# Kernel optimization log

Measured on AMD Instinct MI355X. Metric: run time of the kernel, lower is better.

## Reference

```python
import jax, jax.numpy as jnp
import numpy as np

N_E = 8192
E_DIM = 256
BETA = 0.25


def setup_inputs() -> dict:
    key = jax.random.key(0)
    k1, k2 = jax.random.split(key)
    z = jax.random.normal(k1, (16, 1024, E_DIM), dtype=jnp.float32)
    # matches embedding.weight.data.uniform_(-1/n_e, 1/n_e)
    embedding = jax.random.uniform(k2, (N_E, E_DIM), dtype=jnp.float32,
                                   minval=-1.0 / N_E, maxval=1.0 / N_E)
    return {"z": z, "embedding": embedding}


def reference(z, embedding):
    B, S, D = z.shape  # [16, 1024, 256]
    zf = z.reshape(-1, D)  # [N, D], N = B*S
    # squared L2 distances to every codebook entry: [N, n_e]
    d = (jnp.sum(zf * zf, axis=1, keepdims=True)
         + jnp.sum(embedding * embedding, axis=1)
         - 2.0 * (zf @ embedding.T))
    min_encoding_indices = jnp.argmin(d, axis=1)  # [N]
    # one-hot encodings (returned by the module) [N, n_e]
    min_encodings = jax.nn.one_hot(min_encoding_indices, N_E, dtype=jnp.float32)
    # z_q = min_encodings @ embedding == gather of nearest codes
    z_q = embedding[min_encoding_indices].reshape(z.shape)  # [B, S, D]
    sg = jax.lax.stop_gradient
    loss = jnp.mean((sg(z_q) - z) ** 2) + BETA * jnp.mean((z_q - sg(z)) ** 2)
    # straight-through estimator
    z_q_st = z + sg(z_q - z)
    e_mean = jnp.mean(min_encodings, axis=0)  # [n_e]
    perplexity = jnp.exp(-jnp.sum(e_mean * jnp.log(e_mean + 1e-10)))
    return (loss, z_q_st, perplexity, min_encodings, min_encoding_indices[:, None])
```

## Files before the change

kernel.cpp:

```cpp
#include <hip/hip_runtime.h>
#include <cstddef>

#define NROWS 16384
#define NE    8192
#define DD    256

typedef unsigned long long u64;
typedef float vf4 __attribute__((ext_vector_type(4)));
typedef short bf16x8 __attribute__((ext_vector_type(8)));
typedef float f32x4 __attribute__((ext_vector_type(4)));
typedef unsigned short us8 __attribute__((ext_vector_type(8)));

#define OH_TOT ((size_t)NROWS * NE)
#define OH_VEC ((OH_TOT - 4) / 4)
#define CAND_CAP 4000000
#define LLIST_CAP 2048

__global__ __launch_bounds__(256) void k_rowsq(
    const float* __restrict__ z, const float* __restrict__ emb,
    float* __restrict__ zsq, float* __restrict__ esq,
    u64* __restrict__ best, int* __restrict__ counts,
    float* __restrict__ wadd, int* __restrict__ cand_n,
    unsigned short* __restrict__ ebf)
{
  const int g = blockIdx.x * 256 + threadIdx.x;
  if (g == 0) *cand_n = 0;
  if (g < NE) counts[g] = 0;
  if (g < NROWS) best[g] = ~0ull;

  const float* row;
  float* outp;
  if (g < NROWS) { row = z + (size_t)g * DD;            outp = zsq + g; }
  else           { row = emb + (size_t)(g - NROWS) * DD; outp = esq + (g - NROWS); }

  float sa = 0.0f;
  float half_s[2];
#pragma unroll
  for (int h = 0; h < 2; ++h) {
    const float* p = row + h * 128;
    float r[8];
    {
      const float4 v0 = *(const float4*)(p);
      const float4 v1 = *(const float4*)(p + 4);
      const float xs[8] = {v0.x, v0.y, v0.z, v0.w, v1.x, v1.y, v1.z, v1.w};
#pragma unroll
      for (int j = 0; j < 8; ++j) {
        float sq = xs[j] * xs[j];
        asm volatile("" : "+v"(sq));
        r[j] = sq;
        sa += fabsf(xs[j]);
      }
    }
    for (int i = 8; i < 128; i += 8) {
      const float4 v0 = *(const float4*)(p + i);
      const float4 v1 = *(const float4*)(p + i + 4);
      const float xs[8] = {v0.x, v0.y, v0.z, v0.w, v1.x, v1.y, v1.z, v1.w};
#pragma unroll
      for (int j = 0; j < 8; ++j) {
        float sq = xs[j] * xs[j];
        asm volatile("" : "+v"(sq));
        r[j] = r[j] + sq;
        sa += fabsf(xs[j]);
      }
    }
    half_s[h] = ((r[0] + r[1]) + (r[2] + r[3])) + ((r[4] + r[5]) + (r[6] + r[7]));
  }
  const float zs = half_s[0] + half_s[1];
  *outp = zs;
  if (g < NROWS) {
    wadd[g] = 2.0f * ((zs + 2.0f) * 1.2e-7f + 2.0f * (1.0e-6f * sa) + 5.0e-8f);
  } else {
    const int c = g - NROWS;
    const int t = c >> 4, l = c & 15;
#pragma unroll
    for (int kt = 0; kt < 8; ++kt) {
#pragma unroll
      for (int kq = 0; kq < 4; ++kq) {
        const float4 v0 = *(const float4*)(row + kt * 32 + kq * 8);
        const float4 v1 = *(const float4*)(row + kt * 32 + kq * 8 + 4);
        const float xs[8] = {v0.x, v0.y, v0.z, v0.w, v1.x, v1.y, v1.z, v1.w};
        us8 u;
#pragma unroll
        for (int j = 0; j < 8; ++j) {
          const unsigned b = __float_as_uint(xs[j]);
          u[j] = (unsigned short)((b + 0x7FFFu + ((b >> 16) & 1u)) >> 16);
        }
        *(us8*)(ebf + (((size_t)(t * 8 + kt)) * 64 + kq * 16 + l) * 8) = u;
      }
    }
  }
}

__device__ __forceinline__ unsigned short f2bf_rne(float f) {
  const unsigned u = __float_as_uint(f);
  return (unsigned short)((u + 0x7FFFu + ((u >> 16) & 1u)) >> 16);
}
__device__ __forceinline__ unsigned encf(float f) {
  const unsigned u = __float_as_uint(f);
  return (u & 0x80000000u) ? ~u : (u | 0x80000000u);
}
__device__ __forceinline__ float decf(unsigned k) {
  const unsigned u = (k & 0x80000000u) ? (k ^ 0x80000000u) : ~k;
  return __uint_as_float(u);
}

__global__ __launch_bounds__(256) void k_screen(
    const float* __restrict__ z, const unsigned short* __restrict__ ebf,
    const float* __restrict__ esq, const float* __restrict__ wadd,
    unsigned* __restrict__ cand, int* __restrict__ cand_n,
    float* __restrict__ ohbase)
{
  __shared__ unsigned smin[64];
  __shared__ float wl[64];
  __shared__ unsigned llist[LLIST_CAP];
  __shared__ unsigned lcnt;
  __shared__ unsigned gbase;

  const int tid = threadIdx.x;
  const int b = blockIdx.x;
  const int x = b & 7;
  const int quarter = x >> 1;
  const int panel = (b >> 3) * 2 + (x & 1);
  const int R0 = panel * 64;
  const int C0 = quarter * 2048;
  const int T0 = C0 >> 4;

  const int wave = tid >> 6;
  const int lane = tid & 63;
  const int l15 = lane & 15;
  const int kg = lane >> 4;

  if (tid < 64) { smin[tid] = 0xFFFFFFFFu; wl[tid] = wadd[R0 + tid]; }
  if (tid == 0) lcnt = 0;

  bf16x8 af[8];
  {
    const float* zp_ = z + (size_t)(R0 + wave * 16 + l15) * DD + kg * 8;
#pragma unroll
    for (int kt = 0; kt < 8; ++kt) {
      const float4 a0 = *(const float4*)(zp_ + kt * 32);
      const float4 a1 = *(const float4*)(zp_ + kt * 32 + 4);
      bf16x8 w;
      w[0] = (short)f2bf_rne(a0.x); w[1] = (short)f2bf_rne(a0.y);
      w[2] = (short)f2bf_rne(a0.z); w[3] = (short)f2bf_rne(a0.w);
      w[4] = (short)f2bf_rne(a1.x); w[5] = (short)f2bf_rne(a1.y);
      w[6] = (short)f2bf_rne(a1.z); w[7] = (short)f2bf_rne(a1.w);
      af[kt] = w;
    }
  }
  __syncthreads();

  const int rbase = wave * 16 + kg * 4;
  float wlr[4], thr[4], rm[4];
#pragma unroll
  for (int r = 0; r < 4; ++r) { wlr[r] = wl[rbase + r]; thr[r] = 1e30f; rm[r] = 1e30f; }

#define PUSH(E_)                                                            \
  {                                                                         \
    const unsigned s_ = atomicAdd(&lcnt, 1u);                               \
    if (s_ < LLIST_CAP) llist[s_] = (E_);                                   \
    else { const int g_ = atomicAdd(cand_n, 1);                             \
           if (g_ < CAND_CAP) cand[g_] = (E_); }                            \
  }

#define STEPBODY(S_, EMIT_)                                                 \
  {                                                                         \
    const int t0 = T0 + 2 * (S_);                                           \
    const bf16x8* fb = (const bf16x8*)ebf;                                  \
    bf16x8 b0[8], b1[8];                                                    \
    _Pragma("unroll")                                                       \
    for (int kt = 0; kt < 8; ++kt) {                                        \
      b0[kt] = fb[(size_t)(t0 * 8 + kt) * 64 + lane];                       \
      b1[kt] = fb[(size_t)((t0 + 1) * 8 + kt) * 64 + lane];                 \
    }                                                                       \
    f32x4 e0 = (f32x4){0,0,0,0}, o0 = (f32x4){0,0,0,0};                     \
    f32x4 e1 = (f32x4){0,0,0,0}, o1 = (f32x4){0,0,0,0};                     \
    _Pragma("unroll")                                                       \
    for (int kt = 0; kt < 8; kt += 2) {                                     \
      e0 = __builtin_amdgcn_mfma_f32_16x16x32_bf16(af[kt], b0[kt], e0, 0, 0, 0);         \
      o0 = __builtin_amdgcn_mfma_f32_16x16x32_bf16(af[kt + 1], b0[kt + 1], o0, 0, 0, 0); \
      e1 = __builtin_amdgcn_mfma_f32_16x16x32_bf16(af[kt], b1[kt], e1, 0, 0, 0);         \
      o1 = __builtin_amdgcn_mfma_f32_16x16x32_bf16(af[kt + 1], b1[kt + 1], o1, 0, 0, 0); \
    }                                                                       \
    const int c0 = C0 + (S_) * 32 + l15;                                    \
    const int c1 = c0 + 16;                                                 \
    const float ev0 = esq[c0];                                              \
    const float ev1 = esq[c1];                                              \
    float rv0[4], rv1[4];                                                   \
    float gm = 1e30f;                                                       \
    _Pragma("unroll")                                                       \
    for (int r = 0; r < 4; ++r) {                                           \
      rv0[r] = ev0 - 2.0f * (e0[r] + o0[r]);                                \
      rv1[r] = ev1 - 2.0f * (e1[r] + o1[r]);                                \
      const float mn = fminf(rv0[r], rv1[r]);                               \
      rm[r] = fminf(rm[r], mn);                                             \
      gm = fminf(gm, mn - thr[r]);                                          \
    }                                                                       \
    if ((EMIT_) && gm <= 0.0f) {                                            \
      _Pragma("unroll")                                                     \
      for (int r = 0; r < 4; ++r) {                                         \
        if (rv0[r] <= thr[r]) PUSH(((unsigned)(R0 + rbase + r) << 13) | (unsigned)c0); \
        if (rv1[r] <= thr[r]) PUSH(((unsigned)(R0 + rbase + r) << 13) | (unsigned)c1); \
      }                                                                     \
    }                                                                       \
  }

#define FLUSH_REFRESH                                                       \
  {                                                                         \
    _Pragma("unroll")                                                       \
    for (int r = 0; r < 4; ++r) {                                           \
      float mn = rm[r];                                                     \
      mn = fminf(mn, __shfl_xor(mn, 1, 16));                                \
      mn = fminf(mn, __shfl_xor(mn, 2, 16));                                \
      mn = fminf(mn, __shfl_xor(mn, 4, 16));                                \
      mn = fminf(mn, __shfl_xor(mn, 8, 16));                                \
      if (l15 == 0) atomicMin(&smin[rbase + r], encf(mn));                  \
    }                                                                       \
    _Pragma("unroll")                                                       \
    for (int r = 0; r < 4; ++r) thr[r] = decf(smin[rbase + r]) + wlr[r];    \
  }

#pragma unroll 1
  for (int s = 0; s < 64; ++s) {
    STEPBODY(s, (s >= 2));
    if (s == 1 || (s & 7) == 7) FLUSH_REFRESH;
  }

  __syncthreads();
#pragma unroll
  for (int r = 0; r < 4; ++r) thr[r] = decf(smin[rbase + r]) + wlr[r];
  STEPBODY(0, 1);
  STEPBODY(1, 1);

  __syncthreads();
  const unsigned n = (lcnt < LLIST_CAP) ? lcnt : LLIST_CAP;
  if (tid == 0) gbase = (unsigned)atomicAdd(cand_n, (int)n);
  __syncthreads();
  for (unsigned i = tid; i < n; i += 256) {
    const unsigned g = gbase + i;
    if (g < CAND_CAP) cand[g] = llist[i];
  }

  {
    const vf4 zz = {0.0f, 0.0f, 0.0f, 0.0f};
    float* zp0 = ohbase + 2;
    size_t zt = (size_t)b * 32768 + tid;
#pragma unroll 4
    for (int i = 0; i < 128; ++i) {
      if (zt < OH_VEC) __builtin_nontemporal_store(zz, (vf4*)(zp0 + 4 * zt));
      zt += 256;
    }
    if (b == 0 && tid == 0) { ohbase[0] = 0.0f; ohbase[1] = 0.0f; }
    if (b == 1023 && tid == 0) { ohbase[OH_TOT - 2] = 0.0f; ohbase[OH_TOT - 1] = 0.0f; }
  }
}

__global__ __launch_bounds__(256) void k_recheck(
    const float* __restrict__ z, const float* __restrict__ emb,
    const float* __restrict__ zsq, const float* __restrict__ esq,
    const unsigned* __restrict__ cand, const int* __restrict__ cand_n,
    u64* __restrict__ best)
{
  const int n = min(*cand_n, CAND_CAP);
  for (int i = blockIdx.x * 256 + threadIdx.x; i < n; i += gridDim.x * 256) {
    const unsigned e = cand[i];
    const int row = (int)(e >> 13);
    const int col = (int)(e & (NE - 1));
    const float4* zr = (const float4*)(z + (size_t)row * DD);
    const float4* er = (const float4*)(emb + (size_t)col * DD);
    float dot = 0.0f;
#pragma unroll 8
    for (int q = 0; q < 64; ++q) {
      const float4 a = zr[q];
      const float4 b = er[q];
      dot = fmaf(a.x, b.x, dot);
      dot = fmaf(a.y, b.y, dot);
      dot = fmaf(a.z, b.z, dot);
      dot = fmaf(a.w, b.w, dot);
    }
    const float s1 = zsq[row] + esq[col];
    const float dv = s1 - 2.0f * dot;
    atomicMin(&best[row], ((u64)__float_as_uint(dv) << 32) | (unsigned)col);
  }
}

__global__ __launch_bounds__(256) void k_gather2(
    const float* __restrict__ z, const float* __restrict__ emb,
    const u64* __restrict__ best,
    float* __restrict__ out_zq, float* __restrict__ out_onehot,
    float* __restrict__ out_idx, float* __restrict__ partials,
    int* __restrict__ counts)
{
  __shared__ float sred[256];
  const int row = blockIdx.x * 4 + (threadIdx.x >> 6);
  const int lane = threadIdx.x & 63;
  const int idx = (int)(unsigned)(best[row] & 0xffffffffull);
  const int k0 = lane * 4;

  const float4 e  = *(const float4*)(emb + (size_t)idx * DD + k0);
  const float4 zv = *(const float4*)(z + (size_t)row * DD + k0);
  *(float4*)(out_zq + (size_t)row * DD + k0) = e;

  const float dx = e.x - zv.x, dy = e.y - zv.y, dz = e.z - zv.z, dw = e.w - zv.w;
  sred[threadIdx.x] = dx * dx + dy * dy + dz * dz + dw * dw;

  if (lane == 0) {
    out_idx[row] = (float)idx;
    out_onehot[(size_t)row * NE + idx] = 1.0f;
    atomicAdd(&counts[idx], 1);
  }
  __syncthreads();
  for (int s = 128; s > 0; s >>= 1) {
    if (threadIdx.x < s) sred[threadIdx.x] += sred[threadIdx.x + s];
    __syncthreads();
  }
  if (threadIdx.x == 0) partials[blockIdx.x] = sred[0];
}

__global__ __launch_bounds__(256) void k_final(
    const int* __restrict__ counts, const float* __restrict__ partials,
    float* __restrict__ out_loss, float* __restrict__ out_perp)
{
  __shared__ float sred[256];
  __shared__ float sl[256];
  float le = 0.0f;
  for (int e = threadIdx.x; e < NE; e += 256) {
    const float p = (float)counts[e] * (1.0f / 16384.0f);
    le += p * logf(p + 1e-10f);
  }
  float ll = 0.0f;
  for (int b = threadIdx.x; b < NROWS / 4; b += 256) ll += partials[b];
  sred[threadIdx.x] = le;
  sl[threadIdx.x] = ll;
  __syncthreads();
  for (int s = 128; s > 0; s >>= 1) {
    if (threadIdx.x < s) {
      sred[threadIdx.x] += sred[threadIdx.x + s];
      sl[threadIdx.x] += sl[threadIdx.x + s];
    }
    __syncthreads();
  }
  if (threadIdx.x == 0) {
    *out_perp = expf(-sred[0]);
    *out_loss = sl[0] * (1.25f / 4194304.0f);
  }
}

extern "C" void kernel_launch(void* const* d_in, const int* in_sizes, int n_in,
                              void* d_out, int out_size, void* d_ws, size_t ws_size,
                              hipStream_t stream) {
  const float* z   = (const float*)d_in[0];
  const float* emb = (const float*)d_in[1];

  float* out        = (float*)d_out;
  float* out_loss   = out;
  float* out_zq     = out + 1;
  float* out_perp   = out + 4194305;
  float* out_onehot = out + 4194306;
  float* out_idx    = out + 138412034;

  float* zsq      = (float*)d_ws;
  float* esq      = zsq + NROWS;
  u64*   best     = (u64*)(esq + NE);
  int*   counts   = (int*)(best + NROWS);
  float* partials = (float*)(counts + NE);
  float* wadd     = partials + 4096;
  int*   cand_n   = (int*)(wadd + NROWS);
  unsigned short* ebf = (unsigned short*)(wadd + NROWS + 4);
  unsigned* cand  = (unsigned*)(ebf + (size_t)NE * DD);

  k_rowsq<<<96, 256, 0, stream>>>(z, emb, zsq, esq, best, counts, wadd, cand_n, ebf);
  k_screen<<<1024, 256, 0, stream>>>(z, ebf, esq, wadd, cand, cand_n, out_onehot);
  k_recheck<<<512, 256, 0, stream>>>(z, emb, zsq, esq, cand, cand_n, best);
  k_gather2<<<NROWS / 4, 256, 0, stream>>>(z, emb, best, out_zq, out_onehot,
                                           out_idx, partials, counts);
  k_final<<<1, 256, 0, stream>>>(counts, partials, out_loss, out_perp);
}
```

Before: 1.013 ms.

## Use two-pass min-then-screen in k_screen and split one-hot zeroing into kernel

The screening kernel becomes two passes. The first pass computes each row's exact block-local bf16 minimum over all 2048 columns, and the second pass recomputes the MFMA distances and emits candidates against that final threshold. This replaces the old interleaved refresh-and-emit scheme, which emitted extra candidates early while thresholds were still loose and ran two redo steps at the end. Zeroing the large one-hot output moves into a separate k_zero kernel, and waves_per_eu(3) is set on the screen kernel. The cost is doubled MFMA and codebook-read work in screening and an extra kernel launch, traded for fewer candidates to recheck.

```diff
diff --git a/kernel.cpp b/kernel.cpp
--- a/kernel.cpp
+++ b/kernel.cpp
@@ -104,11 +104,12 @@
   return __uint_as_float(u);
 }
 
-__global__ __launch_bounds__(256) void k_screen(
+__global__ __launch_bounds__(256)
+__attribute__((amdgpu_waves_per_eu(3)))
+void k_screen(
     const float* __restrict__ z, const unsigned short* __restrict__ ebf,
     const float* __restrict__ esq, const float* __restrict__ wadd,
-    unsigned* __restrict__ cand, int* __restrict__ cand_n,
-    float* __restrict__ ohbase)
+    unsigned* __restrict__ cand, int* __restrict__ cand_n)
 {
   __shared__ unsigned smin[64];
   __shared__ float wl[64];
@@ -151,9 +152,40 @@
   __syncthreads();
 
   const int rbase = wave * 16 + kg * 4;
-  float wlr[4], thr[4], rm[4];
-#pragma unroll
-  for (int r = 0; r < 4; ++r) { wlr[r] = wl[rbase + r]; thr[r] = 1e30f; rm[r] = 1e30f; }
+  const bf16x8* fb = (const bf16x8*)ebf;
+
+  float rm[4] = {1e30f, 1e30f, 1e30f, 1e30f};
+#pragma unroll 1
+  for (int tt = 0; tt < 128; ++tt) {
+    bf16x8 bfr[8];
+#pragma unroll
+    for (int kt = 0; kt < 8; ++kt)
+      bfr[kt] = fb[(size_t)((T0 + tt) * 8 + kt) * 64 + lane];
+    f32x4 e = (f32x4){0, 0, 0, 0}, o = (f32x4){0, 0, 0, 0};
+#pragma unroll
+    for (int kt = 0; kt < 8; kt += 2) {
+      e = __builtin_amdgcn_mfma_f32_16x16x32_bf16(af[kt], bfr[kt], e, 0, 0, 0);
+      o = __builtin_amdgcn_mfma_f32_16x16x32_bf16(af[kt + 1], bfr[kt + 1], o, 0, 0, 0);
+    }
+    const float ev = esq[C0 + tt * 16 + l15];
+#pragma unroll
+    for (int r = 0; r < 4; ++r)
+      rm[r] = fminf(rm[r], ev - 2.0f * (e[r] + o[r]));
+  }
+#pragma unroll
+  for (int r = 0; r < 4; ++r) {
+    float mn = rm[r];
+    mn = fminf(mn, __shfl_xor(mn, 1, 16));
+    mn = fminf(mn, __shfl_xor(mn, 2, 16));
+    mn = fminf(mn, __shfl_xor(mn, 4, 16));
+    mn = fminf(mn, __shfl_xor(mn, 8, 16));
+    if (l15 == 0) atomicMin(&smin[rbase + r], encf(mn));
+  }
+  __syncthreads();
+
+  float thr[4];
+#pragma unroll
+  for (int r = 0; r < 4; ++r) thr[r] = decf(smin[rbase + r]) + wl[rbase + r];
 
 #define PUSH(E_)                                                            \
   {                                                                         \
@@ -163,74 +195,33 @@
            if (g_ < CAND_CAP) cand[g_] = (E_); }                            \
   }
 
-#define STEPBODY(S_, EMIT_)                                                 \
-  {                                                                         \
-    const int t0 = T0 + 2 * (S_);                                           \
-    const bf16x8* fb = (const bf16x8*)ebf;                                  \
-    bf16x8 b0[8], b1[8];                                                    \
-    _Pragma("unroll")                                                       \
-    for (int kt = 0; kt < 8; ++kt) {                                        \
-      b0[kt] = fb[(size_t)(t0 * 8 + kt) * 64 + lane];                       \
-      b1[kt] = fb[(size_t)((t0 + 1) * 8 + kt) * 64 + lane];                 \
-    }                                                                       \
-    f32x4 e0 = (f32x4){0,0,0,0}, o0 = (f32x4){0,0,0,0};                     \
-    f32x4 e1 = (f32x4){0,0,0,0}, o1 = (f32x4){0,0,0,0};                     \
-    _Pragma("unroll")                                                       \
-    for (int kt = 0; kt < 8; kt += 2) {                                     \
-      e0 = __builtin_amdgcn_mfma_f32_16x16x32_bf16(af[kt], b0[kt], e0, 0, 0, 0);         \
-      o0 = __builtin_amdgcn_mfma_f32_16x16x32_bf16(af[kt + 1], b0[kt + 1], o0, 0, 0, 0); \
-      e1 = __builtin_amdgcn_mfma_f32_16x16x32_bf16(af[kt], b1[kt], e1, 0, 0, 0);         \
-      o1 = __builtin_amdgcn_mfma_f32_16x16x32_bf16(af[kt + 1], b1[kt + 1], o1, 0, 0, 0); \
-    }                                                                       \
-    const int c0 = C0 + (S_) * 32 + l15;                                    \
-    const int c1 = c0 + 16;                                                 \
-    const float ev0 = esq[c0];                                              \
-    const float ev1 = esq[c1];                                              \
-    float rv0[4], rv1[4];                                                   \
-    float gm = 1e30f;                                                       \
-    _Pragma("unroll")                                                       \
-    for (int r = 0; r < 4; ++r) {                                           \
-      rv0[r] = ev0 - 2.0f * (e0[r] + o0[r]);                                \
-      rv1[r] = ev1 - 2.0f * (e1[r] + o1[r]);                                \
-      const float mn = fminf(rv0[r], rv1[r]);                               \
-      rm[r] = fminf(rm[r], mn);                                             \
-      gm = fminf(gm, mn - thr[r]);                                          \
-    }                                                                       \
-    if ((EMIT_) && gm <= 0.0f) {                                            \
-      _Pragma("unroll")                                                     \
-      for (int r = 0; r < 4; ++r) {                                         \
-        if (rv0[r] <= thr[r]) PUSH(((unsigned)(R0 + rbase + r) << 13) | (unsigned)c0); \
-        if (rv1[r] <= thr[r]) PUSH(((unsigned)(R0 + rbase + r) << 13) | (unsigned)c1); \
-      }                                                                     \
-    }                                                                       \
-  }
-
-#define FLUSH_REFRESH                                                       \
-  {                                                                         \
-    _Pragma("unroll")                                                       \
-    for (int r = 0; r < 4; ++r) {                                           \
-      float mn = rm[r];                                                     \
-      mn = fminf(mn, __shfl_xor(mn, 1, 16));                                \
-      mn = fminf(mn, __shfl_xor(mn, 2, 16));                                \
-      mn = fminf(mn, __shfl_xor(mn, 4, 16));                                \
-      mn = fminf(mn, __shfl_xor(mn, 8, 16));                                \
-      if (l15 == 0) atomicMin(&smin[rbase + r], encf(mn));                  \
-    }                                                                       \
-    _Pragma("unroll")                                                       \
-    for (int r = 0; r < 4; ++r) thr[r] = decf(smin[rbase + r]) + wlr[r];    \
-  }
-
 #pragma unroll 1
-  for (int s = 0; s < 64; ++s) {
-    STEPBODY(s, (s >= 2));
-    if (s == 1 || (s & 7) == 7) FLUSH_REFRESH;
-  }
-
-  __syncthreads();
-#pragma unroll
-  for (int r = 0; r < 4; ++r) thr[r] = decf(smin[rbase + r]) + wlr[r];
-  STEPBODY(0, 1);
-  STEPBODY(1, 1);
+  for (int tt = 0; tt < 128; ++tt) {
+    bf16x8 bfr[8];
+#pragma unroll
+    for (int kt = 0; kt < 8; ++kt)
+      bfr[kt] = fb[(size_t)((T0 + tt) * 8 + kt) * 64 + lane];
+    f32x4 e = (f32x4){0, 0, 0, 0}, o = (f32x4){0, 0, 0, 0};
+#pragma unroll
+    for (int kt = 0; kt < 8; kt += 2) {
+      e = __builtin_amdgcn_mfma_f32_16x16x32_bf16(af[kt], bfr[kt], e, 0, 0, 0);
+      o = __builtin_amdgcn_mfma_f32_16x16x32_bf16(af[kt + 1], bfr[kt + 1], o, 0, 0, 0);
+    }
+    const int c = C0 + tt * 16 + l15;
+    const float ev = esq[c];
+    float rv[4];
+    float gm = 1e30f;
+#pragma unroll
+    for (int r = 0; r < 4; ++r) {
+      rv[r] = ev - 2.0f * (e[r] + o[r]);
+      gm = fminf(gm, rv[r] - thr[r]);
+    }
+    if (gm <= 0.0f) {
+#pragma unroll
+      for (int r = 0; r < 4; ++r)
+        if (rv[r] <= thr[r]) PUSH(((unsigned)(R0 + rbase + r) << 13) | (unsigned)c);
+    }
+  }
 
   __syncthreads();
   const unsigned n = (lcnt < LLIST_CAP) ? lcnt : LLIST_CAP;
@@ -240,18 +231,21 @@
     const unsigned g = gbase + i;
     if (g < CAND_CAP) cand[g] = llist[i];
   }
-
-  {
-    const vf4 zz = {0.0f, 0.0f, 0.0f, 0.0f};
-    float* zp0 = ohbase + 2;
-    size_t zt = (size_t)b * 32768 + tid;
+}
+
+__global__ __launch_bounds__(256) void k_zero(float* __restrict__ ohbase)
+{
+  const vf4 zz = {0.0f, 0.0f, 0.0f, 0.0f};
+  float* zp = ohbase + 2;
+  size_t s = (size_t)blockIdx.x * 16384 + threadIdx.x;
 #pragma unroll 4
-    for (int i = 0; i < 128; ++i) {
-      if (zt < OH_VEC) __builtin_nontemporal_store(zz, (vf4*)(zp0 + 4 * zt));
-      zt += 256;
-    }
-    if (b == 0 && tid == 0) { ohbase[0] = 0.0f; ohbase[1] = 0.0f; }
-    if (b == 1023 && tid == 0) { ohbase[OH_TOT - 2] = 0.0f; ohbase[OH_TOT - 1] = 0.0f; }
+  for (int it = 0; it < 64; ++it) {
+    if (s < OH_VEC) __builtin_nontemporal_store(zz, (vf4*)(zp + 4 * s));
+    s += 256;
+  }
+  if (blockIdx.x == 0 && threadIdx.x == 0) {
+    ohbase[0] = 0.0f; ohbase[1] = 0.0f;
+    ohbase[OH_TOT - 2] = 0.0f; ohbase[OH_TOT - 1] = 0.0f;
   }
 }
 
@@ -370,7 +364,8 @@
   unsigned* cand  = (unsigned*)(ebf + (size_t)NE * DD);
 
   k_rowsq<<<96, 256, 0, stream>>>(z, emb, zsq, esq, best, counts, wadd, cand_n, ebf);
-  k_screen<<<1024, 256, 0, stream>>>(z, ebf, esq, wadd, cand, cand_n, out_onehot);
+  k_screen<<<1024, 256, 0, stream>>>(z, ebf, esq, wadd, cand, cand_n);
+  k_zero<<<2048, 256, 0, stream>>>(out_onehot);
   k_recheck<<<512, 256, 0, stream>>>(z, emb, zsq, esq, cand, cand_n, best);
   k_gather2<<<NROWS / 4, 256, 0, stream>>>(z, emb, best, out_zq, out_onehot,
                                            out_idx, partials, counts);
```

Result: no change. 1.026 ms (+1.3%).
